# Kernel optimization log

Hardware: AMD Instinct MI355X
Metric: run time of the kernel (lower is better)

The kernel has to match this reference:

```python
import jax, jax.numpy as jnp
import numpy as np


def setup_inputs() -> dict:
    key = jax.random.key(0)
    kA, kB = jax.random.split(key)
    B, H, W, C = 8, 48, 48, 256
    feature_A = jax.random.normal(kA, (B, H, W, C), dtype=jnp.float32)
    feature_B = jax.random.normal(kB, (B, H, W, C), dtype=jnp.float32)
    return {"feature_A": feature_A, "feature_B": feature_B}


def reference(feature_A, feature_B):
    # corr[b,i,j,k,l] = mean_c A[b,i,j,c] * B[b,k,l,c]
    # Expressed as a batched GEMM over the channel dim instead of the
    # naive [B,H,W,H,W,C] broadcast intermediate.
    C = feature_A.shape[-1]
    corr = jnp.einsum('bijc,bklc->bijkl', feature_A, feature_B) / C
    # L2 norm over source positions (i,j) per target position (k,l)
    penalty = jnp.sqrt(jnp.sum(corr * corr, axis=(1, 2), keepdims=True))  # [B,1,1,H,W]
    return corr / penalty
```

## Files before the change

### kernel.cpp

```cpp
#include <hip/hip_runtime.h>
#include <hip/hip_bf16.h>


#define HW2 2304
#define CH  256
#define NB  8
#define BK  32
#define LDK 40

typedef __attribute__((ext_vector_type(8))) short bf16x8;
typedef __attribute__((ext_vector_type(4))) float f32x4;

static __device__ inline short f2bf(float f) {
    union { float f; unsigned u; } x; x.f = f;
    unsigned r = x.u + 0x7FFFu + ((x.u >> 16) & 1u);
    return (short)(r >> 16);
}

__global__ __launch_bounds__(256) void corr_gemm(const float* __restrict__ A,
                                                 const float* __restrict__ B,
                                                 float* __restrict__ out,
                                                 float* __restrict__ colSumSq) {
    __shared__ short As[128 * LDK];
    __shared__ short Bs[128 * LDK];
    __shared__ float colSq[128];

    const int tid = threadIdx.x;
    const int bx = blockIdx.x;
    const int by = blockIdx.y;
    const int b  = blockIdx.z;

    if (tid < 128) colSq[tid] = 0.0f;

    const float* Ab = A + ((size_t)b * HW2 + (size_t)by * 128) * CH;
    const float* Bb = B + ((size_t)b * HW2 + (size_t)bx * 128) * CH;

    const int sm = tid >> 3;
    const int sk = (tid & 7) * 4;

    const int wave = tid >> 6;
    const int lane = tid & 63;
    const int wm   = (wave >> 1) * 64;
    const int wn   = (wave & 1) * 64;
    const int lr   = lane & 15;
    const int quad = lane >> 4;
    const int k8   = quad * 8;

    f32x4 acc[4][4];
#pragma unroll
    for (int i = 0; i < 4; i++)
#pragma unroll
        for (int j = 0; j < 4; j++) acc[i][j] = (f32x4){0.f, 0.f, 0.f, 0.f};

    for (int kt = 0; kt < CH; kt += BK) {
#pragma unroll
        for (int r = 0; r < 4; r++) {
            const int row = sm + r * 32;
            float4 va = *(const float4*)(Ab + (size_t)row * CH + kt + sk);
            float4 vb = *(const float4*)(Bb + (size_t)row * CH + kt + sk);
            short4 pa, pb;
            pa.x = f2bf(va.x); pa.y = f2bf(va.y); pa.z = f2bf(va.z); pa.w = f2bf(va.w);
            pb.x = f2bf(vb.x); pb.y = f2bf(vb.y); pb.z = f2bf(vb.z); pb.w = f2bf(vb.w);
            *(short4*)&As[row * LDK + sk] = pa;
            *(short4*)&Bs[row * LDK + sk] = pb;
        }
        __syncthreads();

        bf16x8 af[4], bfr[4];
#pragma unroll
        for (int mt = 0; mt < 4; mt++)
            af[mt] = *(const bf16x8*)&As[(wm + mt * 16 + lr) * LDK + k8];
#pragma unroll
        for (int nt = 0; nt < 4; nt++)
            bfr[nt] = *(const bf16x8*)&Bs[(wn + nt * 16 + lr) * LDK + k8];
#pragma unroll
        for (int mt = 0; mt < 4; mt++)
#pragma unroll
            for (int nt = 0; nt < 4; nt++)
                acc[mt][nt] = __builtin_amdgcn_mfma_f32_16x16x32_bf16(
                    af[mt], bfr[nt], acc[mt][nt], 0, 0, 0);
        __syncthreads();
    }

    const float scale = 1.0f / (float)CH;
    const size_t outBase = (size_t)b * HW2 * HW2;
    const int colBase = bx * 128 + wn;
#pragma unroll
    for (int nt = 0; nt < 4; nt++) {
        const int col = colBase + nt * 16 + lr;
        float s = 0.f;
#pragma unroll
        for (int mt = 0; mt < 4; mt++) {
            const int row0 = by * 128 + wm + mt * 16 + quad * 4;
            f32x4 v = acc[mt][nt];
#pragma unroll
            for (int r = 0; r < 4; r++) {
                float val = v[r] * scale;
                out[outBase + (size_t)(row0 + r) * HW2 + col] = val;
                s += val * val;
            }
        }
        s += __shfl_xor(s, 16);
        s += __shfl_xor(s, 32);
        if (quad == 0) atomicAdd(&colSq[wn + nt * 16 + lr], s);
    }
    __syncthreads();
    if (tid < 128)
        atomicAdd(&colSumSq[(size_t)b * HW2 + bx * 128 + tid], colSq[tid]);
}

__global__ __launch_bounds__(256) void corr_norm(float* __restrict__ out,
                                                 const float* __restrict__ colSumSq) {
    const int n4 = NB * HW2 * (HW2 / 4);
    const int per_b = HW2 * (HW2 / 4);
    for (int i = blockIdx.x * blockDim.x + threadIdx.x; i < n4;
         i += gridDim.x * blockDim.x) {
        const int b = i / per_b;
        const int col = (i * 4) % HW2;
        const float* ss = colSumSq + b * HW2 + col;
        float4 v = ((float4*)out)[i];
        v.x *= rsqrtf(ss[0]);
        v.y *= rsqrtf(ss[1]);
        v.z *= rsqrtf(ss[2]);
        v.w *= rsqrtf(ss[3]);
        ((float4*)out)[i] = v;
    }
}

extern "C" void kernel_launch(void* const* d_in, const int* in_sizes, int n_in,
                              void* d_out, int out_size, void* d_ws, size_t ws_size,
                              hipStream_t stream) {
    const float* A = (const float*)d_in[0];
    const float* B = (const float*)d_in[1];
    float* out = (float*)d_out;
    float* colSumSq = (float*)d_ws;

    hipMemsetAsync(colSumSq, 0, (size_t)NB * HW2 * sizeof(float), stream);

    dim3 grid(HW2 / 128, HW2 / 128, NB);
    corr_gemm<<<grid, 256, 0, stream>>>(A, B, out, colSumSq);

    corr_norm<<<4096, 256, 0, stream>>>(out, colSumSq);
}
```

Baseline: 291.5 us.

## Recompute GEMM in second pass to fuse normalization and pre-convert inputs to bf16

Replaces the write-then-rescale flow with two GEMM passes: the first only accumulates per-column sums of squares, and the second recomputes the correlation and writes normalized output directly. This removes the full read-modify-write of the large output tensor. Inputs are converted to bf16 once in a separate kernel and streamed into LDS with async global-to-LDS copies. The cost is doubled MFMA work, and the unpadded LDS layout may introduce bank conflicts.

Measured after the change: 251.7 us. 1.16x faster.

```diff
diff --git a/kernel.cpp b/kernel.cpp
--- a/kernel.cpp
+++ b/kernel.cpp
@@ -5,24 +5,46 @@
 #define HW2 2304
 #define CH  256
 #define NB  8
-#define BK  32
-#define LDK 40
+#define NELEM (NB * HW2 * CH)
 
 typedef __attribute__((ext_vector_type(8))) short bf16x8;
 typedef __attribute__((ext_vector_type(4))) float f32x4;
 
-static __device__ inline short f2bf(float f) {
+static __device__ inline unsigned short f2bf(float f) {
     union { float f; unsigned u; } x; x.f = f;
     unsigned r = x.u + 0x7FFFu + ((x.u >> 16) & 1u);
-    return (short)(r >> 16);
+    return (unsigned short)(r >> 16);
 }
 
-__global__ __launch_bounds__(256) void corr_gemm(const float* __restrict__ A,
-                                                 const float* __restrict__ B,
-                                                 float* __restrict__ out,
-                                                 float* __restrict__ colSumSq) {
-    __shared__ short As[128 * LDK];
-    __shared__ short Bs[128 * LDK];
+static __device__ inline void async_copy16(const void* g, void* l) {
+    __builtin_amdgcn_global_load_lds(
+        (const __attribute__((address_space(1))) unsigned int*)g,
+        (__attribute__((address_space(3))) unsigned int*)l, 16, 0, 0);
+}
+
+__global__ __launch_bounds__(256) void convert_bf16(const float* __restrict__ A,
+                                                    const float* __restrict__ B,
+                                                    unsigned short* __restrict__ Abf,
+                                                    unsigned short* __restrict__ Bbf) {
+    const int n4 = NELEM / 4;
+    for (int i = blockIdx.x * blockDim.x + threadIdx.x; i < 2 * n4;
+         i += gridDim.x * blockDim.x) {
+        const bool isA = i < n4;
+        const int j = isA ? i : i - n4;
+        float4 v = (isA ? (const float4*)A : (const float4*)B)[j];
+        ushort4 p;
+        p.x = f2bf(v.x); p.y = f2bf(v.y); p.z = f2bf(v.z); p.w = f2bf(v.w);
+        *(ushort4*)((isA ? Abf : Bbf) + (size_t)j * 4) = p;
+    }
+}
+
+template <bool WRITE_OUT>
+__global__ __launch_bounds__(256) void corr_pass(const unsigned short* __restrict__ Abf,
+                                                 const unsigned short* __restrict__ Bbf,
+                                                 float* __restrict__ colSqG,
+                                                 float* __restrict__ out) {
+    __shared__ unsigned short As[128 * 32];
+    __shared__ unsigned short Bs[128 * 32];
     __shared__ float colSq[128];
 
     const int tid = threadIdx.x;
@@ -30,13 +52,13 @@
     const int by = blockIdx.y;
     const int b  = blockIdx.z;
 
-    if (tid < 128) colSq[tid] = 0.0f;
+    if (!WRITE_OUT && tid < 128) colSq[tid] = 0.0f;
 
-    const float* Ab = A + ((size_t)b * HW2 + (size_t)by * 128) * CH;
-    const float* Bb = B + ((size_t)b * HW2 + (size_t)bx * 128) * CH;
+    const unsigned short* Ab = Abf + ((size_t)b * HW2 + (size_t)by * 128) * CH;
+    const unsigned short* Bb = Bbf + ((size_t)b * HW2 + (size_t)bx * 128) * CH;
 
-    const int sm = tid >> 3;
-    const int sk = (tid & 7) * 4;
+    const int srow  = tid >> 2;
+    const int skcol = (tid & 3) * 8;
 
     const int wave = tid >> 6;
     const int lane = tid & 63;
@@ -52,27 +74,23 @@
 #pragma unroll
         for (int j = 0; j < 4; j++) acc[i][j] = (f32x4){0.f, 0.f, 0.f, 0.f};
 
-    for (int kt = 0; kt < CH; kt += BK) {
+    for (int kt = 0; kt < CH; kt += 32) {
 #pragma unroll
-        for (int r = 0; r < 4; r++) {
-            const int row = sm + r * 32;
-            float4 va = *(const float4*)(Ab + (size_t)row * CH + kt + sk);
-            float4 vb = *(const float4*)(Bb + (size_t)row * CH + kt + sk);
-            short4 pa, pb;
-            pa.x = f2bf(va.x); pa.y = f2bf(va.y); pa.z = f2bf(va.z); pa.w = f2bf(va.w);
-            pb.x = f2bf(vb.x); pb.y = f2bf(vb.y); pb.z = f2bf(vb.z); pb.w = f2bf(vb.w);
-            *(short4*)&As[row * LDK + sk] = pa;
-            *(short4*)&Bs[row * LDK + sk] = pb;
+        for (int i = 0; i < 2; i++) {
+            async_copy16(Ab + (size_t)(srow + i * 64) * CH + kt + skcol,
+                         &As[tid * 8 + i * 2048]);
+            async_copy16(Bb + (size_t)(srow + i * 64) * CH + kt + skcol,
+                         &Bs[tid * 8 + i * 2048]);
         }
         __syncthreads();
 
         bf16x8 af[4], bfr[4];
 #pragma unroll
         for (int mt = 0; mt < 4; mt++)
-            af[mt] = *(const bf16x8*)&As[(wm + mt * 16 + lr) * LDK + k8];
+            af[mt] = *(const bf16x8*)&As[(wm + mt * 16 + lr) * 32 + k8];
 #pragma unroll
         for (int nt = 0; nt < 4; nt++)
-            bfr[nt] = *(const bf16x8*)&Bs[(wn + nt * 16 + lr) * LDK + k8];
+            bfr[nt] = *(const bf16x8*)&Bs[(wn + nt * 16 + lr) * 32 + k8];
 #pragma unroll
         for (int mt = 0; mt < 4; mt++)
 #pragma unroll
@@ -82,48 +100,39 @@
         __syncthreads();
     }
 
-    const float scale = 1.0f / (float)CH;
-    const size_t outBase = (size_t)b * HW2 * HW2;
     const int colBase = bx * 128 + wn;
+    if (!WRITE_OUT) {
 #pragma unroll
-    for (int nt = 0; nt < 4; nt++) {
-        const int col = colBase + nt * 16 + lr;
-        float s = 0.f;
+        for (int nt = 0; nt < 4; nt++) {
+            float s = 0.f;
 #pragma unroll
-        for (int mt = 0; mt < 4; mt++) {
-            const int row0 = by * 128 + wm + mt * 16 + quad * 4;
-            f32x4 v = acc[mt][nt];
+            for (int mt = 0; mt < 4; mt++) {
+                f32x4 v = acc[mt][nt];
 #pragma unroll
-            for (int r = 0; r < 4; r++) {
-                float val = v[r] * scale;
-                out[outBase + (size_t)(row0 + r) * HW2 + col] = val;
-                s += val * val;
+                for (int r = 0; r < 4; r++) s += v[r] * v[r];
+            }
+            s += __shfl_xor(s, 16);
+            s += __shfl_xor(s, 32);
+            if (quad == 0) atomicAdd(&colSq[wn + nt * 16 + lr], s);
+        }
+        __syncthreads();
+        if (tid < 128)
+            atomicAdd(&colSqG[(size_t)b * HW2 + bx * 128 + tid], colSq[tid]);
+    } else {
+        const size_t outBase = (size_t)b * HW2 * HW2;
+#pragma unroll
+        for (int nt = 0; nt < 4; nt++) {
+            const int col = colBase + nt * 16 + lr;
+            const float rinv = rsqrtf(colSqG[(size_t)b * HW2 + col]);
+#pragma unroll
+            for (int mt = 0; mt < 4; mt++) {
+                const int row0 = by * 128 + wm + mt * 16 + quad * 4;
+                f32x4 v = acc[mt][nt];
+#pragma unroll
+                for (int r = 0; r < 4; r++)
+                    out[outBase + (size_t)(row0 + r) * HW2 + col] = v[r] * rinv;
             }
         }
-        s += __shfl_xor(s, 16);
-        s += __shfl_xor(s, 32);
-        if (quad == 0) atomicAdd(&colSq[wn + nt * 16 + lr], s);
-    }
-    __syncthreads();
-    if (tid < 128)
-        atomicAdd(&colSumSq[(size_t)b * HW2 + bx * 128 + tid], colSq[tid]);
-}
-
-__global__ __launch_bounds__(256) void corr_norm(float* __restrict__ out,
-                                                 const float* __restrict__ colSumSq) {
-    const int n4 = NB * HW2 * (HW2 / 4);
-    const int per_b = HW2 * (HW2 / 4);
-    for (int i = blockIdx.x * blockDim.x + threadIdx.x; i < n4;
-         i += gridDim.x * blockDim.x) {
-        const int b = i / per_b;
-        const int col = (i * 4) % HW2;
-        const float* ss = colSumSq + b * HW2 + col;
-        float4 v = ((float4*)out)[i];
-        v.x *= rsqrtf(ss[0]);
-        v.y *= rsqrtf(ss[1]);
-        v.z *= rsqrtf(ss[2]);
-        v.w *= rsqrtf(ss[3]);
-        ((float4*)out)[i] = v;
     }
 }
 
@@ -133,12 +142,15 @@
     const float* A = (const float*)d_in[0];
     const float* B = (const float*)d_in[1];
     float* out = (float*)d_out;
-    float* colSumSq = (float*)d_ws;
 
-    hipMemsetAsync(colSumSq, 0, (size_t)NB * HW2 * sizeof(float), stream);
+    unsigned short* Abf = (unsigned short*)d_ws;
+    unsigned short* Bbf = Abf + NELEM;
+    float* colSqG = (float*)(Bbf + NELEM);
+
+    hipMemsetAsync(colSqG, 0, (size_t)NB * HW2 * sizeof(float), stream);
+    convert_bf16<<<2048, 256, 0, stream>>>(A, B, Abf, Bbf);
 
     dim3 grid(HW2 / 128, HW2 / 128, NB);
-    corr_gemm<<<grid, 256, 0, stream>>>(A, B, out, colSumSq);
-
-    corr_norm<<<4096, 256, 0, stream>>>(out, colSumSq);
+    corr_pass<false><<<grid, 256, 0, stream>>>(Abf, Bbf, colSqG, out);
+    corr_pass<true><<<grid, 256, 0, stream>>>(Abf, Bbf, colSqG, out);
 }
```
